# Optimization experiments

Hardware: AMD Instinct MI355X
Metric: run time of the kernel (lower is better)

The kernel has to match this reference:

```python
import jax, jax.numpy as jnp
import numpy as np

B, S, D, K = 8, 2048, 1024, 204  # K = int(0.1 * seq_len)
LN_EPS = 1e-12


def setup_inputs() -> dict:
    key = jax.random.key(0)
    ks = jax.random.split(key, 8)
    scale = 0.02
    return {
        "input_tensor": jax.random.normal(ks[0], (B, S, D), jnp.float32),
        "attention_mask": jnp.zeros((B, 1, 1, S), jnp.float32),  # unused by module
        "Wq": jax.random.normal(ks[1], (D, K), jnp.float32) * scale,
        "bq": jnp.zeros((K,), jnp.float32),
        "Wk": jax.random.normal(ks[2], (D, K), jnp.float32) * scale,
        "bk": jnp.zeros((K,), jnp.float32),
        "Wv": jax.random.normal(ks[3], (D, D), jnp.float32) * scale,
        "bv": jnp.zeros((D,), jnp.float32),
        "Wd": jax.random.normal(ks[4], (D, D), jnp.float32) * scale,
        "bd": jnp.zeros((D,), jnp.float32),
        "gamma": jnp.ones((D,), jnp.float32),
        "beta": jnp.zeros((D,), jnp.float32),
    }


def reference(input_tensor, attention_mask, Wq, bq, Wk, bk, Wv, bv, Wd, bd, gamma, beta):
    # factorized synthesizer: low-rank (k=204) Q/K projections
    q = input_tensor @ Wq + bq          # [B,S,K]
    k = input_tensor @ Wk + bk          # [B,S,K]
    v = input_tensor @ Wv + bv          # [B,S,D]
    scores = jnp.einsum('bsk,btk->bst', q, k)          # [B,S,S]
    probs = jax.nn.softmax(scores, axis=-1)
    # per-head matmul with broadcast probs == direct matmul on merged heads
    ctx = jnp.einsum('bst,btd->bsd', probs, v)          # [B,S,D]
    h = ctx @ Wd + bd
    y = h + input_tensor                                 # residual
    mean = jnp.mean(y, axis=-1, keepdims=True)
    var = jnp.mean(jnp.square(y - mean), axis=-1, keepdims=True)
    return gamma * (y - mean) / jnp.sqrt(var + LN_EPS) + beta
```

## Files before the change

kernel.cpp:

```cpp
#include <hip/hip_runtime.h>
#include <stdint.h>

#define BB 8
#define SS 2048
#define DD 1024
#define KREAL 204
#define KP 256
#define BM 128
#define BK 64

typedef __attribute__((ext_vector_type(8))) short short8;
typedef __attribute__((ext_vector_type(4))) float floatx4;
typedef uint16_t u16;
typedef uint32_t u32;

__device__ __forceinline__ float bf2f(u16 u) {
    union { float f; u32 i; } c; c.i = ((u32)u) << 16; return c.f;
}
__device__ __forceinline__ u16 f2bf(float f) {
    union { float f; u32 i; } c; c.f = f;
    u32 i = c.i;
    u32 r = (i + 0x7FFFu + ((i >> 16) & 1u)) >> 16;
    return (u16)r;
}

union V16 { uint4 u; short8 s8; u16 h[8]; };

#if defined(__has_builtin)
#if __has_builtin(__builtin_amdgcn_global_load_lds)
#define HAVE_GLL 1
#endif
#endif

__device__ __forceinline__ void gload16(const u16* g, u16* l) {
#ifdef HAVE_GLL
    __builtin_amdgcn_global_load_lds(
        (const __attribute__((address_space(1))) void*)(uintptr_t)g,
        (__attribute__((address_space(3))) void*)(u32)(uintptr_t)(void*)l,
        16, 0, 0);
#else
    *(uint4*)l = *(const uint4*)g;
#endif
}

__device__ __forceinline__ void stage_tile(const u16* __restrict__ src, size_t ld,
                                           u16* lds, int tid) {
#pragma unroll
    for (int j = 0; j < 4; j++) {
        int flat = j * 256 + tid;
        int row = flat >> 3, slot = flat & 7;
        int kg = slot ^ (row & 7);
        gload16(src + (size_t)row * ld + kg * 8, lds + flat * 8);
    }
}

__device__ __forceinline__ short8 frag(const u16* lds, int row, int kslot) {
    return *(const short8*)&lds[(row << 6) + (((kslot ^ (row & 7)) & 7) << 3)];
}

__device__ __forceinline__ void mfma_step(const u16* As, const u16* Bs,
                                          int wm, int wn, int ln, int quad,
                                          floatx4 acc[4][4]) {
#pragma unroll
    for (int kk = 0; kk < 2; kk++) {
        short8 av[4], bv[4];
#pragma unroll
        for (int mt = 0; mt < 4; mt++) av[mt] = frag(As, wm * 64 + mt * 16 + ln, kk * 4 + quad);
#pragma unroll
        for (int nt = 0; nt < 4; nt++) bv[nt] = frag(Bs, wn * 64 + nt * 16 + ln, kk * 4 + quad);
#pragma unroll
        for (int mt = 0; mt < 4; mt++)
#pragma unroll
            for (int nt = 0; nt < 4; nt++)
                acc[mt][nt] = __builtin_amdgcn_mfma_f32_16x16x32_bf16(av[mt], bv[nt], acc[mt][nt], 0, 0, 0);
    }
}

__global__ __launch_bounds__(256) void k_cast_bf16(
    const float* __restrict__ x, u16* __restrict__ o) {
    size_t i = ((size_t)blockIdx.x * 256 + threadIdx.x) * 4;
    float4 v = *(const float4*)&x[i];
    ushort4 p;
    p.x = f2bf(v.x); p.y = f2bf(v.y); p.z = f2bf(v.z); p.w = f2bf(v.w);
    *(ushort4*)&o[i] = p;
}

__global__ __launch_bounds__(256) void k_prep_weights(
    const float* __restrict__ Wq, const float* __restrict__ Wk,
    const float* __restrict__ Wv, const float* __restrict__ Wd,
    u16* __restrict__ Wqkt, u16* __restrict__ Wv16, u16* __restrict__ Wdt) {
    const int z = blockIdx.z;
    __shared__ u16 tile[32][33];
    int k0 = blockIdx.x * 32, n0 = blockIdx.y * 32;
    int tx = threadIdx.x & 31, ty = threadIdx.x >> 5;
    if (z == 2) {
        for (int i = ty; i < 32; i += 8) {
            size_t idx = (size_t)(k0 + i) * 1024 + n0 + tx;
            Wv16[idx] = f2bf(Wv[idx]);
        }
        return;
    }
    const float* W; u16* out; int N, Npad, rowoff;
    if (z == 0)      { W = Wq; out = Wqkt; N = KREAL; Npad = 256;  rowoff = 0;   }
    else if (z == 1) { W = Wk; out = Wqkt; N = KREAL; Npad = 256;  rowoff = 256; }
    else             { W = Wd; out = Wdt;  N = 1024;  Npad = 1024; rowoff = 0;   }
    if (n0 >= Npad) return;
    for (int i = ty; i < 32; i += 8) {
        int n = n0 + tx;
        tile[i][tx] = (n < N) ? f2bf(W[(size_t)(k0 + i) * N + n]) : (u16)0;
    }
    __syncthreads();
    for (int i = ty; i < 32; i += 8) {
        int n = n0 + i;
        if (n < Npad) out[(size_t)(rowoff + n) * 1024 + k0 + tx] = tile[tx][i];
    }
}

__global__ __launch_bounds__(256) void k_prep_bias(
    const float* __restrict__ bv, const float* __restrict__ bd,
    const float* __restrict__ Wd, const float* __restrict__ bq,
    const float* __restrict__ bk, float* __restrict__ bc,
    float* __restrict__ bqk) {
    const int t = threadIdx.x;
    if (blockIdx.x < 16) {
        __shared__ float red[4][64];
        int n = blockIdx.x * 64 + (t & 63);
        int dc = t >> 6;
        float s = 0.f;
        for (int d = dc * 256; d < dc * 256 + 256; d++)
            s += bv[d] * Wd[(size_t)d * 1024 + n];
        red[dc][t & 63] = s;
        __syncthreads();
        if (dc == 0) bc[n] = bd[n] + red[0][t & 63] + red[1][t & 63] + red[2][t & 63] + red[3][t & 63];
    } else {
        for (int i = t; i < 512; i += 256) {
            float v = 0.f;
            if (i < KREAL) v = bq[i];
            else if (i >= 256 && i < 256 + KREAL) v = bk[i - 256];
            bqk[i] = v;
        }
    }
}

__global__ __launch_bounds__(256) void k_gemm_proj(
    const u16* __restrict__ A, const u16* __restrict__ Wt,
    const float* __restrict__ bias, int nbias,
    u16* __restrict__ C, int ldc, int kiters, int mode) {
    __shared__ u16 As[BM * BK];
    __shared__ u16 Bs[BM * BK];
    const int tid = threadIdx.x;
    const int m0 = blockIdx.x * BM, n0 = blockIdx.y * BM;
    const int lane = tid & 63, w = tid >> 6;
    const int wm = w >> 1, wn = w & 1;
    const int ln = lane & 15, quad = lane >> 4;
    const size_t K = (size_t)kiters * BK;

    floatx4 acc[4][4];
    floatx4 zero = {0.f, 0.f, 0.f, 0.f};
#pragma unroll
    for (int mt = 0; mt < 4; mt++)
#pragma unroll
        for (int nt = 0; nt < 4; nt++) acc[mt][nt] = zero;

    const u16* Ab = A + (size_t)m0 * K;
    const u16* Bb = Wt + (size_t)n0 * K;
    for (int kt = 0; kt < kiters; kt++) {
        __syncthreads();
        stage_tile(Ab + kt * BK, K, As, tid);
        stage_tile(Bb + kt * BK, K, Bs, tid);
        __syncthreads();
        mfma_step(As, Bs, wm, wn, ln, quad, acc);
    }

#pragma unroll
    for (int mt = 0; mt < 4; mt++) {
        const int row0 = m0 + wm * 64 + mt * 16 + quad * 4;
#pragma unroll
        for (int nt = 0; nt < 4; nt++) {
            const int col = n0 + wn * 64 + nt * 16 + ln;
            const float bv = (col < nbias) ? bias[col] : 0.f;
            if (mode == 1) {
                int b = row0 >> 11, s = row0 & 2047;
                ushort4 pk;
                pk.x = f2bf(acc[mt][nt][0] + bv);
                pk.y = f2bf(acc[mt][nt][1] + bv);
                pk.z = f2bf(acc[mt][nt][2] + bv);
                pk.w = f2bf(acc[mt][nt][3] + bv);
                *reinterpret_cast<ushort4*>(&C[((size_t)b << 21) + ((size_t)col << 11) + s]) = pk;
            } else if (mode == 3) {
                ushort4 pk;
                pk.x = f2bf(acc[mt][nt][0] + bv);
                pk.y = f2bf(acc[mt][nt][1] + bv);
                pk.z = f2bf(acc[mt][nt][2] + bv);
                pk.w = f2bf(acc[mt][nt][3] + bv);
                *reinterpret_cast<ushort4*>(&C[(size_t)col * ldc + row0]) = pk;
            } else {
#pragma unroll
                for (int r = 0; r < 4; r++)
                    C[(size_t)(row0 + r) * ldc + col] = f2bf(acc[mt][nt][r] + bv);
            }
        }
    }
}

__global__ __launch_bounds__(256) void k_gemm_qk(
    const u16* __restrict__ qkp, u16* __restrict__ P, float* __restrict__ lg) {
    __shared__ u16 As[BM * BK];
    __shared__ u16 Bs[BM * BK];
    const int tid = threadIdx.x;
    const int s0 = blockIdx.x * BM, t0 = blockIdx.y * BM, bb = blockIdx.z;
    const int lane = tid & 63, w = tid >> 6;
    const int wm = w >> 1, wn = w & 1;
    const int ln = lane & 15, quad = lane >> 4;

    floatx4 acc[4][4];
    floatx4 zero = {0.f, 0.f, 0.f, 0.f};
#pragma unroll
    for (int mt = 0; mt < 4; mt++)
#pragma unroll
        for (int nt = 0; nt < 4; nt++) acc[mt][nt] = zero;

    const u16* Ab = qkp + ((size_t)bb * SS + s0) * 512;
    const u16* Bb = qkp + ((size_t)bb * SS + t0) * 512 + 256;
#pragma unroll
    for (int kt = 0; kt < KP / BK; kt++) {
        __syncthreads();
        stage_tile(Ab + kt * BK, 512, As, tid);
        stage_tile(Bb + kt * BK, 512, Bs, tid);
        __syncthreads();
        mfma_step(As, Bs, wm, wn, ln, quad, acc);
    }

    u16* Pb = P + (size_t)bb * SS * SS;
#pragma unroll
    for (int mt = 0; mt < 4; mt++) {
        const int row0 = s0 + wm * 64 + mt * 16 + quad * 4;
#pragma unroll
        for (int r = 0; r < 4; r++) {
            float rs = 0.f;
#pragma unroll
            for (int nt = 0; nt < 4; nt++) {
                const int col = t0 + wn * 64 + nt * 16 + ln;
                float p = __expf(acc[mt][nt][r] - 30.f);
                rs += p;
                Pb[(size_t)(row0 + r) * SS + col] = f2bf(p);
            }
            rs += __shfl_xor(rs, 1);
            rs += __shfl_xor(rs, 2);
            rs += __shfl_xor(rs, 4);
            rs += __shfl_xor(rs, 8);
            if (ln == 0) atomicAdd(&lg[bb * SS + row0 + r], rs);
        }
    }
}

__global__ __launch_bounds__(256) void k_gemm_h(
    const u16* __restrict__ P, const u16* __restrict__ ut,
    const float* __restrict__ lg, const float* __restrict__ bc,
    const float* __restrict__ xres, u16* __restrict__ y) {
    __shared__ u16 As[BM * BK];
    __shared__ u16 Bs[BM * BK];
    const int tid = threadIdx.x;
    const int s0 = blockIdx.x * BM, d0 = blockIdx.y * BM, bb = blockIdx.z;
    const int lane = tid & 63, w = tid >> 6;
    const int wm = w >> 1, wn = w & 1;
    const int ln = lane & 15, quad = lane >> 4;

    floatx4 acc[4][4];
    floatx4 zero = {0.f, 0.f, 0.f, 0.f};
#pragma unroll
    for (int mt = 0; mt < 4; mt++)
#pragma unroll
        for (int nt = 0; nt < 4; nt++) acc[mt][nt] = zero;

    const u16* Ab = P + ((size_t)bb * SS + s0) * SS;
    const u16* Bb = ut + ((size_t)bb * DD + d0) * SS;
    for (int kt = 0; kt < SS / BK; kt++) {
        __syncthreads();
        stage_tile(Ab + kt * BK, SS, As, tid);
        stage_tile(Bb + kt * BK, SS, Bs, tid);
        __syncthreads();
        mfma_step(As, Bs, wm, wn, ln, quad, acc);
    }

#pragma unroll
    for (int mt = 0; mt < 4; mt++) {
        const int row0 = s0 + wm * 64 + mt * 16 + quad * 4;
#pragma unroll
        for (int r = 0; r < 4; r++) {
            const size_t grow = (size_t)bb * SS + row0 + r;
            const float inv = 1.f / lg[grow];
#pragma unroll
            for (int nt = 0; nt < 4; nt++) {
                const int col = d0 + wn * 64 + nt * 16 + ln;
                y[grow * DD + col] = f2bf(acc[mt][nt][r] * inv + bc[col] + xres[grow * DD + col]);
            }
        }
    }
}

__global__ __launch_bounds__(256) void k_layernorm(
    const u16* __restrict__ y, const float* __restrict__ gamma,
    const float* __restrict__ beta, float* __restrict__ out) {
    const int tid = threadIdx.x;
    const int lane = tid & 63, w = tid >> 6;
    const size_t row = (size_t)blockIdx.x * 4 + w;
    const u16* yr = y + row * DD;

    float v[16];
#pragma unroll
    for (int j = 0; j < 2; j++) {
        V16 t;
        t.u = *(const uint4*)&yr[j * 512 + lane * 8];
#pragma unroll
        for (int e = 0; e < 8; e++) v[j * 8 + e] = bf2f(t.h[e]);
    }
    float s = 0.f, sq = 0.f;
#pragma unroll
    for (int i = 0; i < 16; i++) { s += v[i]; sq += v[i] * v[i]; }
#pragma unroll
    for (int msk = 1; msk < 64; msk <<= 1) {
        s  += __shfl_xor(s,  msk, 64);
        sq += __shfl_xor(sq, msk, 64);
    }
    float mean = s * (1.f / 1024.f);
    float var  = sq * (1.f / 1024.f) - mean * mean;
    float rstd = rsqrtf(fmaxf(var, 0.f) + 1e-12f);
#pragma unroll
    for (int j = 0; j < 2; j++) {
        int cbase = j * 512 + lane * 8;
#pragma unroll
        for (int h = 0; h < 2; h++) {
            float4 g  = *(const float4*)&gamma[cbase + h * 4];
            float4 bt = *(const float4*)&beta [cbase + h * 4];
            float4 o;
            o.x = g.x * (v[j * 8 + h * 4 + 0] - mean) * rstd + bt.x;
            o.y = g.y * (v[j * 8 + h * 4 + 1] - mean) * rstd + bt.y;
            o.z = g.z * (v[j * 8 + h * 4 + 2] - mean) * rstd + bt.z;
            o.w = g.w * (v[j * 8 + h * 4 + 3] - mean) * rstd + bt.w;
            *(float4*)&out[row * DD + cbase + h * 4] = o;
        }
    }
}

extern "C" void kernel_launch(void* const* d_in, const int* in_sizes, int n_in,
                              void* d_out, int out_size, void* d_ws, size_t ws_size,
                              hipStream_t stream) {
    const float* x     = (const float*)d_in[0];
    const float* Wq    = (const float*)d_in[2];
    const float* bq    = (const float*)d_in[3];
    const float* Wk    = (const float*)d_in[4];
    const float* bk    = (const float*)d_in[5];
    const float* Wv    = (const float*)d_in[6];
    const float* bv    = (const float*)d_in[7];
    const float* Wd    = (const float*)d_in[8];
    const float* bd    = (const float*)d_in[9];
    const float* gamma = (const float*)d_in[10];
    const float* beta  = (const float*)d_in[11];
    float* out = (float*)d_out;

    char* ws = (char*)d_ws;
    u16*   qkp  = (u16*)(ws + 0);
    u16*   ut   = (u16*)(ws + (16u << 20));
    u16*   x16  = (u16*)(ws + (48u << 20));
    u16*   P    = (u16*)(ws + (48u << 20));
    u16*   Wv16 = (u16*)(ws + (80u << 20));
    u16*   Wvdt = (u16*)(ws + (80u << 20) + 2097152);
    u16*   y    = (u16*)(ws + (80u << 20));
    float* lg   = (float*)(ws + 117440512);
    float* bc   = (float*)(ws + 117506048);
    float* bqk  = (float*)(ws + 117510144);
    u16*   Wqkt = (u16*)(ws + 117512192);
    u16*   Wdt  = (u16*)(ws + 118560768);

    dim3 blk(256);

    k_cast_bf16<<<dim3(16384), blk, 0, stream>>>(x, x16);
    k_prep_weights<<<dim3(32, 32, 4), blk, 0, stream>>>(Wq, Wk, Wv, Wd, Wqkt, Wv16, Wdt);
    k_prep_bias<<<dim3(17), blk, 0, stream>>>(bv, bd, Wd, bq, bk, bc, bqk);

    k_gemm_proj<<<dim3(8, 8), blk, 0, stream>>>(Wv16, Wdt, nullptr, 0, Wvdt, 1024, 16, 3);

    k_gemm_proj<<<dim3(128, 4), blk, 0, stream>>>(x16, Wqkt, bqk, 512, qkp, 512, 16, 0);
    k_gemm_proj<<<dim3(128, 8), blk, 0, stream>>>(x16, Wvdt, nullptr, 0, ut, 0, 16, 1);

    hipMemsetAsync(lg, 0, (size_t)BB * SS * sizeof(float), stream);

    for (int g = 0; g < 2; g++) {
        const size_t qo = (size_t)g * 4 * SS * 512;
        const size_t uo = (size_t)g * 4 * (size_t)DD * SS;
        const size_t yo = (size_t)g * 4 * (size_t)SS * DD;
        const size_t lo = (size_t)g * 4 * SS;
        k_gemm_qk<<<dim3(16, 16, 4), blk, 0, stream>>>(qkp + qo, P, lg + lo);
        k_gemm_h <<<dim3(16, 8, 4),  blk, 0, stream>>>(P, ut + uo, lg + lo, bc, x + yo, y + yo);
    }

    k_layernorm<<<dim3(4096), blk, 0, stream>>>(y, gamma, beta, out);
}
```

Measured before the change: 426.0 us.

## Stage GEMM epilogues through LDS for coalesced stores and merge small launches

GEMM epilogues (QK probabilities, H output, projections) now write accumulator tiles into shared memory in two halves and then issue coalesced 16-byte global stores, replacing scattered 2-byte writes. The bias prep kernel is folded into the weight prep kernel, and the Q/K and V projection GEMMs are merged into one launch. The Wv*Wd fold uses a 64x64-tile kernel for more blocks. This targets store inefficiency and launch overhead, at the cost of extra barriers and LDS traffic in each epilogue.

```diff
diff --git a/kernel.cpp b/kernel.cpp
--- a/kernel.cpp
+++ b/kernel.cpp
@@ -43,8 +43,8 @@
 #endif
 }
 
-__device__ __forceinline__ void stage_tile(const u16* __restrict__ src, size_t ld,
-                                           u16* lds, int tid) {
+__device__ __forceinline__ void stage128(const u16* __restrict__ src, size_t ld,
+                                         u16* lds, int tid) {
 #pragma unroll
     for (int j = 0; j < 4; j++) {
         int flat = j * 256 + tid;
@@ -53,6 +53,16 @@
         gload16(src + (size_t)row * ld + kg * 8, lds + flat * 8);
     }
 }
+__device__ __forceinline__ void stage64(const u16* __restrict__ src, size_t ld,
+                                        u16* lds, int tid) {
+#pragma unroll
+    for (int j = 0; j < 2; j++) {
+        int flat = j * 256 + tid;
+        int row = flat >> 3, slot = flat & 7;
+        int kg = slot ^ (row & 7);
+        gload16(src + (size_t)row * ld + kg * 8, lds + flat * 8);
+    }
+}
 
 __device__ __forceinline__ short8 frag(const u16* lds, int row, int kslot) {
     return *(const short8*)&lds[(row << 6) + (((kslot ^ (row & 7)) & 7) << 3)];
@@ -73,6 +83,59 @@
 #pragma unroll
             for (int nt = 0; nt < 4; nt++)
                 acc[mt][nt] = __builtin_amdgcn_mfma_f32_16x16x32_bf16(av[mt], bv[nt], acc[mt][nt], 0, 0, 0);
+    }
+}
+
+template <typename F>
+__device__ __forceinline__ void store_rowmajor_128(
+    u16* smem, u16* gbase, size_t ldc, int wm, int quad, int ln, int wn,
+    int tid, F valfn) {
+    for (int half = 0; half < 2; half++) {
+        __syncthreads();
+        if (wm == half) {
+#pragma unroll
+            for (int mt = 0; mt < 4; mt++)
+#pragma unroll
+                for (int nt = 0; nt < 4; nt++)
+#pragma unroll
+                    for (int r = 0; r < 4; r++)
+                        smem[(mt * 16 + quad * 4 + r) * 136 + wn * 64 + nt * 16 + ln] =
+                            valfn(mt, nt, r);
+        }
+        __syncthreads();
+#pragma unroll
+        for (int it = 0; it < 4; it++) {
+            int g = it * 256 + tid;
+            int row = g >> 4, tch = g & 15;
+            uint4 v = *(const uint4*)&smem[row * 136 + tch * 8];
+            *(uint4*)&gbase[(size_t)(half * 64 + row) * ldc + tch * 8] = v;
+        }
+    }
+}
+
+template <typename F4>
+__device__ __forceinline__ void store_transposed_128(
+    u16* smem, u16* gbase, size_t ldg, int wm, int wn, int ln, int quad,
+    int tid, F4 valfn4) {
+    for (int half = 0; half < 2; half++) {
+        __syncthreads();
+        if (wn == half) {
+#pragma unroll
+            for (int mt = 0; mt < 4; mt++)
+#pragma unroll
+                for (int nt = 0; nt < 4; nt++) {
+                    ushort4 v = valfn4(mt, nt);
+                    *(ushort4*)&smem[(nt * 16 + ln) * 136 + wm * 64 + mt * 16 + quad * 4] = v;
+                }
+        }
+        __syncthreads();
+#pragma unroll
+        for (int it = 0; it < 4; it++) {
+            int g = it * 256 + tid;
+            int c = g >> 4, sch = g & 15;
+            uint4 v = *(const uint4*)&smem[c * 136 + sch * 8];
+            *(uint4*)&gbase[(size_t)(half * 64 + c) * ldg + sch * 8] = v;
+        }
     }
 }
 
@@ -85,14 +148,40 @@
     *(ushort4*)&o[i] = p;
 }
 
-__global__ __launch_bounds__(256) void k_prep_weights(
+__global__ __launch_bounds__(256) void k_prep(
     const float* __restrict__ Wq, const float* __restrict__ Wk,
     const float* __restrict__ Wv, const float* __restrict__ Wd,
-    u16* __restrict__ Wqkt, u16* __restrict__ Wv16, u16* __restrict__ Wdt) {
+    const float* __restrict__ bv, const float* __restrict__ bd,
+    const float* __restrict__ bq, const float* __restrict__ bk,
+    u16* __restrict__ Wqkt, u16* __restrict__ Wv16, u16* __restrict__ Wdt,
+    float* __restrict__ bc, float* __restrict__ bqk) {
     const int z = blockIdx.z;
+    const int t = threadIdx.x;
+    if (z == 4) {
+        int id = blockIdx.y * 32 + blockIdx.x;
+        if (id < 16) {
+            __shared__ float red[4][64];
+            int n = id * 64 + (t & 63);
+            int dc = t >> 6;
+            float s = 0.f;
+            for (int d = dc * 256; d < dc * 256 + 256; d++)
+                s += bv[d] * Wd[(size_t)d * 1024 + n];
+            red[dc][t & 63] = s;
+            __syncthreads();
+            if (dc == 0) bc[n] = bd[n] + red[0][t & 63] + red[1][t & 63] + red[2][t & 63] + red[3][t & 63];
+        } else if (id == 16) {
+            for (int i = t; i < 512; i += 256) {
+                float v = 0.f;
+                if (i < KREAL) v = bq[i];
+                else if (i >= 256 && i < 256 + KREAL) v = bk[i - 256];
+                bqk[i] = v;
+            }
+        }
+        return;
+    }
     __shared__ u16 tile[32][33];
     int k0 = blockIdx.x * 32, n0 = blockIdx.y * 32;
-    int tx = threadIdx.x & 31, ty = threadIdx.x >> 5;
+    int tx = t & 31, ty = t >> 5;
     if (z == 2) {
         for (int i = ty; i < 32; i += 8) {
             size_t idx = (size_t)(k0 + i) * 1024 + n0 + tx;
@@ -116,44 +205,62 @@
     }
 }
 
-__global__ __launch_bounds__(256) void k_prep_bias(
-    const float* __restrict__ bv, const float* __restrict__ bd,
-    const float* __restrict__ Wd, const float* __restrict__ bq,
-    const float* __restrict__ bk, float* __restrict__ bc,
-    float* __restrict__ bqk) {
-    const int t = threadIdx.x;
-    if (blockIdx.x < 16) {
-        __shared__ float red[4][64];
-        int n = blockIdx.x * 64 + (t & 63);
-        int dc = t >> 6;
-        float s = 0.f;
-        for (int d = dc * 256; d < dc * 256 + 256; d++)
-            s += bv[d] * Wd[(size_t)d * 1024 + n];
-        red[dc][t & 63] = s;
-        __syncthreads();
-        if (dc == 0) bc[n] = bd[n] + red[0][t & 63] + red[1][t & 63] + red[2][t & 63] + red[3][t & 63];
-    } else {
-        for (int i = t; i < 512; i += 256) {
-            float v = 0.f;
-            if (i < KREAL) v = bq[i];
-            else if (i >= 256 && i < 256 + KREAL) v = bk[i - 256];
-            bqk[i] = v;
-        }
-    }
-}
-
-__global__ __launch_bounds__(256) void k_gemm_proj(
-    const u16* __restrict__ A, const u16* __restrict__ Wt,
-    const float* __restrict__ bias, int nbias,
-    u16* __restrict__ C, int ldc, int kiters, int mode) {
-    __shared__ u16 As[BM * BK];
-    __shared__ u16 Bs[BM * BK];
+__global__ __launch_bounds__(256) void k_gemm64(
+    const u16* __restrict__ A, const u16* __restrict__ Bt,
+    u16* __restrict__ C, int ldc) {
+    __shared__ u16 As[64 * 64];
+    __shared__ u16 Bs[64 * 64];
     const int tid = threadIdx.x;
-    const int m0 = blockIdx.x * BM, n0 = blockIdx.y * BM;
+    const int m0 = blockIdx.x * 64, n0 = blockIdx.y * 64;
+    const int lane = tid & 63, w = tid >> 6;
+    const int ln = lane & 15, quad = lane >> 4;
+
+    floatx4 acc[4];
+    floatx4 zero = {0.f, 0.f, 0.f, 0.f};
+#pragma unroll
+    for (int nt = 0; nt < 4; nt++) acc[nt] = zero;
+
+    for (int kt = 0; kt < 16; kt++) {
+        __syncthreads();
+        stage64(A + (size_t)m0 * 1024 + kt * 64, 1024, As, tid);
+        stage64(Bt + (size_t)n0 * 1024 + kt * 64, 1024, Bs, tid);
+        __syncthreads();
+#pragma unroll
+        for (int kk = 0; kk < 2; kk++) {
+            short8 av = frag(As, w * 16 + ln, kk * 4 + quad);
+#pragma unroll
+            for (int nt = 0; nt < 4; nt++) {
+                short8 bvf = frag(Bs, nt * 16 + ln, kk * 4 + quad);
+                acc[nt] = __builtin_amdgcn_mfma_f32_16x16x32_bf16(av, bvf, acc[nt], 0, 0, 0);
+            }
+        }
+    }
+    const int row0 = m0 + w * 16 + quad * 4;
+#pragma unroll
+    for (int nt = 0; nt < 4; nt++) {
+        const int col = n0 + nt * 16 + ln;
+        ushort4 pk;
+        pk.x = f2bf(acc[nt][0]); pk.y = f2bf(acc[nt][1]);
+        pk.z = f2bf(acc[nt][2]); pk.w = f2bf(acc[nt][3]);
+        *reinterpret_cast<ushort4*>(&C[(size_t)col * ldc + row0]) = pk;
+    }
+}
+
+__global__ __launch_bounds__(256) void k_proj(
+    const u16* __restrict__ A, const u16* __restrict__ Wqkt,
+    const u16* __restrict__ Wvdt, const float* __restrict__ bqk,
+    u16* __restrict__ qkp, u16* __restrict__ ut) {
+    __shared__ u16 smem[2 * BM * BK];
+    u16* As = smem; u16* Bs = smem + BM * BK;
+    const int tid = threadIdx.x;
+    const int m0 = blockIdx.x * BM;
+    const int by = blockIdx.y;
     const int lane = tid & 63, w = tid >> 6;
     const int wm = w >> 1, wn = w & 1;
     const int ln = lane & 15, quad = lane >> 4;
-    const size_t K = (size_t)kiters * BK;
+
+    const int n0 = (by < 4) ? by * 128 : (by - 4) * 128;
+    const u16* Bb = (by < 4) ? (Wqkt + (size_t)n0 * 1024) : (Wvdt + (size_t)n0 * 1024);
 
     floatx4 acc[4][4];
     floatx4 zero = {0.f, 0.f, 0.f, 0.f};
@@ -162,51 +269,39 @@
 #pragma unroll
         for (int nt = 0; nt < 4; nt++) acc[mt][nt] = zero;
 
-    const u16* Ab = A + (size_t)m0 * K;
-    const u16* Bb = Wt + (size_t)n0 * K;
-    for (int kt = 0; kt < kiters; kt++) {
-        __syncthreads();
-        stage_tile(Ab + kt * BK, K, As, tid);
-        stage_tile(Bb + kt * BK, K, Bs, tid);
+    const u16* Ab = A + (size_t)m0 * 1024;
+    for (int kt = 0; kt < 16; kt++) {
+        __syncthreads();
+        stage128(Ab + kt * BK, 1024, As, tid);
+        stage128(Bb + kt * BK, 1024, Bs, tid);
         __syncthreads();
         mfma_step(As, Bs, wm, wn, ln, quad, acc);
     }
 
-#pragma unroll
-    for (int mt = 0; mt < 4; mt++) {
-        const int row0 = m0 + wm * 64 + mt * 16 + quad * 4;
-#pragma unroll
-        for (int nt = 0; nt < 4; nt++) {
-            const int col = n0 + wn * 64 + nt * 16 + ln;
-            const float bv = (col < nbias) ? bias[col] : 0.f;
-            if (mode == 1) {
-                int b = row0 >> 11, s = row0 & 2047;
+    if (by < 4) {
+        u16* gbase = qkp + (size_t)m0 * 512 + n0;
+        store_rowmajor_128(smem, gbase, 512, wm, quad, ln, wn, tid,
+            [&](int mt, int nt, int r) -> u16 {
+                int col = n0 + wn * 64 + nt * 16 + ln;
+                return f2bf(acc[mt][nt][r] + bqk[col]);
+            });
+    } else {
+        int b = m0 >> 11, s0loc = m0 & 2047;
+        u16* gbase = ut + ((size_t)b * DD + n0) * SS + s0loc;
+        store_transposed_128(smem, gbase, SS, wm, wn, ln, quad, tid,
+            [&](int mt, int nt) -> ushort4 {
                 ushort4 pk;
-                pk.x = f2bf(acc[mt][nt][0] + bv);
-                pk.y = f2bf(acc[mt][nt][1] + bv);
-                pk.z = f2bf(acc[mt][nt][2] + bv);
-                pk.w = f2bf(acc[mt][nt][3] + bv);
-                *reinterpret_cast<ushort4*>(&C[((size_t)b << 21) + ((size_t)col << 11) + s]) = pk;
-            } else if (mode == 3) {
-                ushort4 pk;
-                pk.x = f2bf(acc[mt][nt][0] + bv);
-                pk.y = f2bf(acc[mt][nt][1] + bv);
-                pk.z = f2bf(acc[mt][nt][2] + bv);
-                pk.w = f2bf(acc[mt][nt][3] + bv);
-                *reinterpret_cast<ushort4*>(&C[(size_t)col * ldc + row0]) = pk;
-            } else {
-#pragma unroll
-                for (int r = 0; r < 4; r++)
-                    C[(size_t)(row0 + r) * ldc + col] = f2bf(acc[mt][nt][r] + bv);
-            }
-        }
+                pk.x = f2bf(acc[mt][nt][0]); pk.y = f2bf(acc[mt][nt][1]);
+                pk.z = f2bf(acc[mt][nt][2]); pk.w = f2bf(acc[mt][nt][3]);
+                return pk;
+            });
     }
 }
 
 __global__ __launch_bounds__(256) void k_gemm_qk(
     const u16* __restrict__ qkp, u16* __restrict__ P, float* __restrict__ lg) {
-    __shared__ u16 As[BM * BK];
-    __shared__ u16 Bs[BM * BK];
+    __shared__ u16 smem[2 * BM * BK];
+    u16* As = smem; u16* Bs = smem + BM * BK;
     const int tid = threadIdx.x;
     const int s0 = blockIdx.x * BM, t0 = blockIdx.y * BM, bb = blockIdx.z;
     const int lane = tid & 63, w = tid >> 6;
@@ -225,26 +320,19 @@
 #pragma unroll
     for (int kt = 0; kt < KP / BK; kt++) {
         __syncthreads();
-        stage_tile(Ab + kt * BK, 512, As, tid);
-        stage_tile(Bb + kt * BK, 512, Bs, tid);
+        stage128(Ab + kt * BK, 512, As, tid);
+        stage128(Bb + kt * BK, 512, Bs, tid);
         __syncthreads();
         mfma_step(As, Bs, wm, wn, ln, quad, acc);
     }
 
-    u16* Pb = P + (size_t)bb * SS * SS;
 #pragma unroll
     for (int mt = 0; mt < 4; mt++) {
         const int row0 = s0 + wm * 64 + mt * 16 + quad * 4;
 #pragma unroll
         for (int r = 0; r < 4; r++) {
-            float rs = 0.f;
-#pragma unroll
-            for (int nt = 0; nt < 4; nt++) {
-                const int col = t0 + wn * 64 + nt * 16 + ln;
-                float p = __expf(acc[mt][nt][r] - 30.f);
-                rs += p;
-                Pb[(size_t)(row0 + r) * SS + col] = f2bf(p);
-            }
+            float rs = __expf(acc[mt][0][r] - 30.f) + __expf(acc[mt][1][r] - 30.f)
+                     + __expf(acc[mt][2][r] - 30.f) + __expf(acc[mt][3][r] - 30.f);
             rs += __shfl_xor(rs, 1);
             rs += __shfl_xor(rs, 2);
             rs += __shfl_xor(rs, 4);
@@ -252,14 +340,20 @@
             if (ln == 0) atomicAdd(&lg[bb * SS + row0 + r], rs);
         }
     }
+
+    u16* gbase = P + (size_t)bb * SS * SS + (size_t)s0 * SS + t0;
+    store_rowmajor_128(smem, gbase, SS, wm, quad, ln, wn, tid,
+        [&](int mt, int nt, int r) -> u16 {
+            return f2bf(__expf(acc[mt][nt][r] - 30.f));
+        });
 }
 
 __global__ __launch_bounds__(256) void k_gemm_h(
     const u16* __restrict__ P, const u16* __restrict__ ut,
     const float* __restrict__ lg, const float* __restrict__ bc,
     const float* __restrict__ xres, u16* __restrict__ y) {
-    __shared__ u16 As[BM * BK];
-    __shared__ u16 Bs[BM * BK];
+    __shared__ u16 smem[2 * BM * BK];
+    u16* As = smem; u16* Bs = smem + BM * BK;
     const int tid = threadIdx.x;
     const int s0 = blockIdx.x * BM, d0 = blockIdx.y * BM, bb = blockIdx.z;
     const int lane = tid & 63, w = tid >> 6;
@@ -277,26 +371,21 @@
     const u16* Bb = ut + ((size_t)bb * DD + d0) * SS;
     for (int kt = 0; kt < SS / BK; kt++) {
         __syncthreads();
-        stage_tile(Ab + kt * BK, SS, As, tid);
-        stage_tile(Bb + kt * BK, SS, Bs, tid);
+        stage128(Ab + kt * BK, SS, As, tid);
+        stage128(Bb + kt * BK, SS, Bs, tid);
         __syncthreads();
         mfma_step(As, Bs, wm, wn, ln, quad, acc);
     }
 
-#pragma unroll
-    for (int mt = 0; mt < 4; mt++) {
-        const int row0 = s0 + wm * 64 + mt * 16 + quad * 4;
-#pragma unroll
-        for (int r = 0; r < 4; r++) {
-            const size_t grow = (size_t)bb * SS + row0 + r;
-            const float inv = 1.f / lg[grow];
-#pragma unroll
-            for (int nt = 0; nt < 4; nt++) {
-                const int col = d0 + wn * 64 + nt * 16 + ln;
-                y[grow * DD + col] = f2bf(acc[mt][nt][r] * inv + bc[col] + xres[grow * DD + col]);
-            }
-        }
-    }
+    u16* gbase = y + ((size_t)bb * SS + s0) * DD + d0;
+    store_rowmajor_128(smem, gbase, DD, wm, quad, ln, wn, tid,
+        [&](int mt, int nt, int r) -> u16 {
+            int rowl = wm * 64 + mt * 16 + quad * 4 + r;
+            size_t grow = (size_t)bb * SS + s0 + rowl;
+            int col = d0 + wn * 64 + nt * 16 + ln;
+            float inv = 1.f / lg[grow];
+            return f2bf(acc[mt][nt][r] * inv + bc[col] + xres[grow * DD + col]);
+        });
 }
 
 __global__ __launch_bounds__(256) void k_layernorm(
@@ -376,13 +465,12 @@
     dim3 blk(256);
 
     k_cast_bf16<<<dim3(16384), blk, 0, stream>>>(x, x16);
-    k_prep_weights<<<dim3(32, 32, 4), blk, 0, stream>>>(Wq, Wk, Wv, Wd, Wqkt, Wv16, Wdt);
-    k_prep_bias<<<dim3(17), blk, 0, stream>>>(bv, bd, Wd, bq, bk, bc, bqk);
-
-    k_gemm_proj<<<dim3(8, 8), blk, 0, stream>>>(Wv16, Wdt, nullptr, 0, Wvdt, 1024, 16, 3);
-
-    k_gemm_proj<<<dim3(128, 4), blk, 0, stream>>>(x16, Wqkt, bqk, 512, qkp, 512, 16, 0);
-    k_gemm_proj<<<dim3(128, 8), blk, 0, stream>>>(x16, Wvdt, nullptr, 0, ut, 0, 16, 1);
+    k_prep<<<dim3(32, 32, 5), blk, 0, stream>>>(Wq, Wk, Wv, Wd, bv, bd, bq, bk,
+                                                Wqkt, Wv16, Wdt, bc, bqk);
+
+    k_gemm64<<<dim3(16, 16), blk, 0, stream>>>(Wv16, Wdt, Wvdt, 1024);
+
+    k_proj<<<dim3(128, 12), blk, 0, stream>>>(x16, Wqkt, Wvdt, bqk, qkp, ut);
 
     hipMemsetAsync(lg, 0, (size_t)BB * SS * sizeof(float), stream);
 
```

After: 384.7 us. 1.11x faster.
